# Performance work log

Hardware: AMD Instinct MI355X
Metric: run time of the kernel (lower is better)

Reference implementation:

```python
import jax, jax.numpy as jnp
import numpy as np

EPS = 1e-5

def conv2d(x, w, b, pad):
    # x: [B,C,H,W], w: [O,I,kh,kw] (OIHW), b: [O]
    y = jax.lax.conv_general_dilated(x, w, (1, 1), [(pad, pad), (pad, pad)],
                                     dimension_numbers=('NCHW', 'OIHW', 'NCHW'))
    return y + b[None, :, None, None]

def bn(x, g, b, m, v):
    # eval-mode BatchNorm2d
    scale = (g / jnp.sqrt(v + EPS))[None, :, None, None]
    return (x - m[None, :, None, None]) * scale + b[None, :, None, None]


def setup_inputs() -> dict:
    key = jax.random.key(0)
    ks = jax.random.split(key, 16)
    B, C, H, W = 2, 64, 64, 64
    Cq = C // 8
    f = lambda k, shp, s=0.05: jax.random.normal(k, shp, dtype=jnp.float32) * s
    return {
        'x': jax.random.normal(ks[0], (B, C, H, W), dtype=jnp.float32),
        'sW': f(ks[1], (C, C, 3, 3)), 'sb': f(ks[2], (C,)),
        's_g': jnp.ones((C,), jnp.float32), 's_b': jnp.zeros((C,), jnp.float32),
        's_m': jnp.zeros((C,), jnp.float32), 's_v': jnp.ones((C,), jnp.float32),
        'cW': f(ks[3], (C, C, 3, 3)), 'cb': f(ks[4], (C,)),
        'c_g': jnp.ones((C,), jnp.float32), 'c_b': jnp.zeros((C,), jnp.float32),
        'c_m': jnp.zeros((C,), jnp.float32), 'c_v': jnp.ones((C,), jnp.float32),
        'qW': f(ks[5], (Cq, C, 1, 1)), 'qb': f(ks[6], (Cq,)),
        'kW': f(ks[7], (Cq, C, 1, 1)), 'kb': f(ks[8], (Cq,)),
        'vW': f(ks[9], (C, C, 1, 1)), 'vb': f(ks[10], (C,)),
        'oW': f(ks[11], (C, C, 1, 1)), 'ob': f(ks[12], (C,)),
        's_gamma': jnp.array([0.5], jnp.float32),
        'c_gamma': jnp.array([0.5], jnp.float32),
    }


def reference(x, sW, sb, s_g, s_b, s_m, s_v, cW, cb, c_g, c_b, c_m, c_v,
              qW, qb, kW, kb, vW, vb, oW, ob, s_gamma, c_gamma):
    # ---- spatial attention branch ----
    s_x = jax.nn.relu(bn(conv2d(x, sW, sb, 1), s_g, s_b, s_m, s_v))  # [B,C,H,W]
    B, C, H, W = s_x.shape
    HW = H * W
    q = conv2d(x, qW, qb, 0).reshape(B, -1, HW)  # [B, C/8, HW]
    k = conv2d(x, kW, kb, 0).reshape(B, -1, HW)  # [B, C/8, HW]
    v = conv2d(x, vW, vb, 0).reshape(B, C, HW)   # [B, C,   HW]
    # aff[b,i,j] = q_i . k_j ; softmax over j (unscaled, per original)
    A = jax.nn.softmax(jnp.einsum('bdi,bdj->bij', q, k), axis=-1)  # [B,HW,HW]
    sa = jnp.einsum('bcj,bij->bci', v, A).reshape(B, C, H, W)
    sa_map = s_gamma[0] * sa + s_x
    # ---- channel attention branch ----
    c_x = jax.nn.relu(bn(conv2d(x, cW, cb, 1), c_g, c_b, c_m, c_v))  # [B,C,H,W]
    fmap = c_x.reshape(B, C, HW)
    Ac = jnp.einsum('bin,bjn->bij', fmap, fmap)  # [B,C,C]
    Ac = jax.nn.softmax(jnp.max(Ac, axis=-1, keepdims=True) - Ac, axis=-1)
    ca = jnp.einsum('bij,bjn->bin', Ac, fmap).reshape(B, C, H, W)
    ca_map = c_gamma[0] * ca + c_x
    # ---- fuse + output adaptor ----
    return conv2d(sa_map + ca_map, oW, ob, 0)
```

## Files before the change

### kernel.cpp

```cpp
#include <hip/hip_runtime.h>

#define HW 4096

typedef __attribute__((ext_vector_type(8)))  short short8;
typedef __attribute__((ext_vector_type(16))) float float16;

__device__ __forceinline__ unsigned short f2bf(float f) {
    unsigned u = __float_as_uint(f);
    u += 0x7fffu + ((u >> 16) & 1u);
    return (unsigned short)(u >> 16);
}

__global__ __launch_bounds__(256) void k_wprep(
    const float* __restrict__ sW, const float* __restrict__ cW,
    const float* __restrict__ sb, const float* __restrict__ cb,
    const float* __restrict__ s_g, const float* __restrict__ s_b,
    const float* __restrict__ s_m, const float* __restrict__ s_v,
    const float* __restrict__ c_g, const float* __restrict__ c_b,
    const float* __restrict__ c_m, const float* __restrict__ c_v,
    const float* __restrict__ oW,
    unsigned short* __restrict__ Wa, float* __restrict__ scsh,
    float* __restrict__ oWTg)
{
    int bx = blockIdx.x;
    int t = threadIdx.x;
    if (bx < 18) {
        int which = bx / 9, khw = bx % 9;
        const float* W = which ? cW : sW;
#pragma unroll
        for (int i = 0; i < 16; i++) {
            int idx = t + 256 * i;
            int oc = idx >> 6, ic = idx & 63;
            float v = W[(size_t)(oc * 64 + ic) * 9 + khw];
            Wa[((size_t)(which * 9 + khw) * 64 + oc) * 64 + ic] = f2bf(v);
        }
        if (bx == 0 && t < 128) {
            int wh = t >> 6, oc = t & 63;
            const float* g  = wh ? c_g : s_g;
            const float* bb = wh ? c_b : s_b;
            const float* m  = wh ? c_m : s_m;
            const float* vv = wh ? c_v : s_v;
            const float* cbias = wh ? cb : sb;
            float scale = g[oc] * rsqrtf(vv[oc] + 1e-5f);
            scsh[wh * 128 + oc]      = scale;
            scsh[wh * 128 + 64 + oc] = (cbias[oc] - m[oc]) * scale + bb[oc];
        }
    } else {
#pragma unroll
        for (int k = 0; k < 16; k++) {
            int idx = t + 256 * k;
            int c = idx >> 6, o = idx & 63;
            oWTg[idx] = oW[(size_t)o * 64 + c];
        }
    }
}

__global__ __launch_bounds__(256, 3) void k_conv_qkv(
    const float* __restrict__ x, const unsigned short* __restrict__ Wa,
    const float* __restrict__ scsh,
    const float* __restrict__ qW, const float* __restrict__ qb,
    const float* __restrict__ kW, const float* __restrict__ kb,
    const float* __restrict__ vW, const float* __restrict__ vb,
    float* __restrict__ sx, float* __restrict__ cx,
    unsigned short* __restrict__ qT, unsigned short* __restrict__ kT,
    unsigned short* __restrict__ vB)
{
    __shared__ unsigned short xs[3 * 8 * 66 * 8];
    int bx = blockIdx.x;
    int t = threadIdx.x;

    if (bx < 256) {
        int which = bx >> 7;
        int b     = (bx >> 6) & 1;
        int row   = bx & 63;
        const float* xb = x + (size_t)(b * 64) * HW;

#pragma unroll
        for (int it = 0; it < 6; it++) {
            int idx  = t + 256 * it;
            int col4 = idx & 15;
            int icp  = (idx >> 4) & 31;
            int lr   = idx >> 9;
            int ir   = row - 1 + lr;
            float fa[4] = {0.f, 0.f, 0.f, 0.f};
            float fb[4] = {0.f, 0.f, 0.f, 0.f};
            if (ir >= 0 && ir < 64) {
                const float* p0 = xb + (size_t)(icp * 2) * HW + ir * 64 + col4 * 4;
                float4 v0 = *(const float4*)p0;
                float4 v1 = *(const float4*)(p0 + HW);
                fa[0] = v0.x; fa[1] = v0.y; fa[2] = v0.z; fa[3] = v0.w;
                fb[0] = v1.x; fb[1] = v1.y; fb[2] = v1.z; fb[3] = v1.w;
            }
            int icg = icp >> 2, io = icp & 3;
#pragma unroll
            for (int j = 0; j < 4; j++) {
                unsigned pack = (unsigned)f2bf(fa[j]) | ((unsigned)f2bf(fb[j]) << 16);
                *(unsigned*)&xs[(((lr * 8 + icg) * 66 + col4 * 4 + j + 1) * 8) + io * 2] = pack;
            }
        }
        if (t < 192) {
            int pair = t & 3;
            int colsel = (t >> 2) & 1;
            int rg = t >> 3;
            *(unsigned*)&xs[((rg * 66 + colsel * 65) * 8) + pair * 2] = 0u;
        }
        __syncthreads();

        int lane = t & 63, w = t >> 6;
        int l31 = lane & 31, half = lane >> 5;
        int colh = w & 1;
        int m0   = (w >> 1) * 32;
        int c    = colh * 32 + l31;

        float16 acc;
#pragma unroll
        for (int i = 0; i < 16; i++) acc[i] = 0.f;

        const unsigned short* Wbase =
            Wa + ((size_t)which * 9) * 4096 + (size_t)(m0 + l31) * 64 + half * 8;

#pragma unroll
        for (int khw = 0; khw < 9; khw++) {
            const int kh = khw / 3, kw = khw % 3;
#pragma unroll
            for (int icq = 0; icq < 4; icq++) {
                short8 af = *(const short8*)(Wbase + (size_t)khw * 4096 + icq * 16);
                const unsigned short* bp =
                    &xs[((kh * 8 + icq * 2 + half) * 66 + kw) * 8];
                short8 bf = *(const short8*)(bp + (size_t)c * 8);
                acc = __builtin_amdgcn_mfma_f32_32x32x16_bf16(af, bf, acc, 0, 0, 0);
            }
        }

        float* out = (which ? cx : sx) + (size_t)(b * 64) * HW;
        const float* sc = scsh + which * 128;
        int hwbase = row * 64 + c;
#pragma unroll
        for (int r = 0; r < 16; r++) {
            int oc = m0 + (r & 3) + 8 * (r >> 2) + 4 * half;
            float s  = sc[oc];
            float sh = sc[64 + oc];
            out[(size_t)oc * HW + hwbase] = fmaxf(acc[r] * s + sh, 0.f);
        }
    } else {
        int ubx = bx - 256;
        int b = ubx / 80, rem = ubx % 80;
        int chunk = rem / 5, g = rem % 5;
        int hw = chunk * 256 + t;
        const float* xb = x + (size_t)(b * 64) * HW + hw;

        float acc[16];
#pragma unroll
        for (int u = 0; u < 16; u++) acc[u] = 0.f;

        if (g == 0) {
            for (int ic = 0; ic < 64; ic++) {
                float xv = xb[ic * HW];
#pragma unroll
                for (int u = 0; u < 8; u++) acc[u]     += qW[u * 64 + ic] * xv;
#pragma unroll
                for (int u = 0; u < 8; u++) acc[8 + u] += kW[u * 64 + ic] * xv;
            }
            short8 qv, kv;
#pragma unroll
            for (int u = 0; u < 8; u++) qv[u] = (short)f2bf(acc[u] + qb[u]);
#pragma unroll
            for (int u = 0; u < 8; u++) kv[u] = (short)f2bf(acc[8 + u] + kb[u]);
            *(short8*)(qT + ((size_t)(b * HW) + hw) * 8) = qv;
            *(short8*)(kT + ((size_t)(b * HW) + hw) * 8) = kv;
        } else {
            int c0 = (g - 1) * 16;
            for (int ic = 0; ic < 64; ic++) {
                float xv = xb[ic * HW];
#pragma unroll
                for (int u = 0; u < 16; u++) acc[u] += vW[(c0 + u) * 64 + ic] * xv;
            }
            int m  = hw & 15;
            int sg = (m & 3) | ((m & 4) << 1) | ((m & 8) >> 1);
            size_t base = ((size_t)(b * 256) + (hw >> 4)) * 1024 + sg;
#pragma unroll
            for (int u = 0; u < 16; u++)
                vB[base + (size_t)(c0 + u) * 16] = f2bf(acc[u] + vb[c0 + u]);
        }
    }
}

union SmemKB {
    struct { float o_sh[4][64][33]; float den_sh[4][32]; } a;
    float slab[64][68];
};

__global__ __launch_bounds__(256, 4) void k_attn_gram(
    const unsigned short* __restrict__ qT, const unsigned short* __restrict__ kT,
    const unsigned short* __restrict__ vB, const float* __restrict__ cx,
    float* __restrict__ Opart, float* __restrict__ denp,
    float* __restrict__ Gpart)
{
    __shared__ SmemKB sm;
    int bx = blockIdx.x;
    int t = threadIdx.x;

    if (bx < 1024) {
        int lane = t & 63, w = t >> 6;
        int half = lane >> 5, l31 = lane & 31;
        int b  = bx >> 9;
        int itile = (bx >> 2) & 127;
        int jh = bx & 3;
        int i0 = itile * 32;

        short8 qf;
        if (half == 0) {
            qf = *(const short8*)(qT + ((size_t)(b * HW) + i0 + l31) * 8);
        } else {
#pragma unroll
            for (int i = 0; i < 8; i++) qf[i] = 0;
        }

        float16 o0, o1;
#pragma unroll
        for (int i = 0; i < 16; i++) { o0[i] = 0.f; o1[i] = 0.f; }
        float denr = 0.f;

        const unsigned short* kTb = kT + (size_t)(b * HW) * 8;
        const unsigned short* vBb = vB + (size_t)b * (256 * 1024);

        for (int tile = 0; tile < 8; tile++) {
            int j0 = jh * 1024 + w * 256 + tile * 32;
            int g0 = j0 >> 4;

            short8 kf;
            if (half == 0) {
                kf = *(const short8*)(kTb + (size_t)(j0 + l31) * 8);
            } else {
#pragma unroll
                for (int i = 0; i < 8; i++) kf[i] = 0;
            }

            float16 z;
#pragma unroll
            for (int i = 0; i < 16; i++) z[i] = 0.f;
            float16 s = __builtin_amdgcn_mfma_f32_32x32x16_bf16(kf, qf, z, 0, 0, 0);

            float pr[16];
#pragma unroll
            for (int r = 0; r < 16; r++) {
                pr[r] = __expf(s[r]);
                denr += pr[r];
            }
            short8 pa0, pa1;
#pragma unroll
            for (int r = 0; r < 8; r++) {
                pa0[r] = (short)f2bf(pr[r]);
                pa1[r] = (short)f2bf(pr[8 + r]);
            }

            const unsigned short* vg0 = vBb + (size_t)g0 * 1024 + half * 8;
            short8 v00 = *(const short8*)(vg0 + (size_t)l31 * 16);
            short8 v01 = *(const short8*)(vg0 + (size_t)(32 + l31) * 16);
            short8 v10 = *(const short8*)(vg0 + 1024 + (size_t)l31 * 16);
            short8 v11 = *(const short8*)(vg0 + 1024 + (size_t)(32 + l31) * 16);

            o0 = __builtin_amdgcn_mfma_f32_32x32x16_bf16(pa0, v00, o0, 0, 0, 0);
            o1 = __builtin_amdgcn_mfma_f32_32x32x16_bf16(pa0, v01, o1, 0, 0, 0);
            o0 = __builtin_amdgcn_mfma_f32_32x32x16_bf16(pa1, v10, o0, 0, 0, 0);
            o1 = __builtin_amdgcn_mfma_f32_32x32x16_bf16(pa1, v11, o1, 0, 0, 0);
        }

        float dfull = denr + __shfl_xor(denr, 32);
        if (half == 0) sm.a.den_sh[w][l31] = dfull;
#pragma unroll
        for (int r = 0; r < 16; r++) {
            int il = (r & 3) + 8 * (r >> 2) + 4 * half;
            sm.a.o_sh[w][l31][il]      = o0[r];
            sm.a.o_sh[w][32 + l31][il] = o1[r];
        }
        __syncthreads();

        int i  = t & 31;
        int cg = t >> 5;
        if (cg == 0)
            denp[jh * 8192 + b * 4096 + i0 + i] =
                sm.a.den_sh[0][i] + sm.a.den_sh[1][i] +
                sm.a.den_sh[2][i] + sm.a.den_sh[3][i];
#pragma unroll
        for (int u = 0; u < 8; u++) {
            int c = cg * 8 + u;
            float sv = sm.a.o_sh[0][c][i] + sm.a.o_sh[1][c][i]
                     + sm.a.o_sh[2][c][i] + sm.a.o_sh[3][c][i];
            Opart[((size_t)(jh * 2 + b) * 64 + c) * HW + i0 + i] = sv;
        }
    } else {
        int gbx = bx - 1024;
        int b = gbx >> 5, slice = gbx & 31;
        int i0 = (t & 15) * 4, j0c = (t >> 4) * 4;
        float acc[4][4] = {};
#pragma unroll
        for (int ch = 0; ch < 2; ch++) {
            int hwb = slice * 128 + ch * 64;
            __syncthreads();
#pragma unroll
            for (int it = 0; it < 16; it++) {
                int idx = t + 256 * it;
                int hw = idx & 63, c = idx >> 6;
                sm.slab[hw][c] = cx[(size_t)(b * 64 + c) * HW + hwb + hw];
            }
            __syncthreads();
#pragma unroll 8
            for (int hw = 0; hw < 64; hw++) {
                float4 ai = *(const float4*)&sm.slab[hw][i0];
                float4 aj = *(const float4*)&sm.slab[hw][j0c];
                acc[0][0] += ai.x * aj.x; acc[0][1] += ai.x * aj.y;
                acc[0][2] += ai.x * aj.z; acc[0][3] += ai.x * aj.w;
                acc[1][0] += ai.y * aj.x; acc[1][1] += ai.y * aj.y;
                acc[1][2] += ai.y * aj.z; acc[1][3] += ai.y * aj.w;
                acc[2][0] += ai.z * aj.x; acc[2][1] += ai.z * aj.y;
                acc[2][2] += ai.z * aj.z; acc[2][3] += ai.z * aj.w;
                acc[3][0] += ai.w * aj.x; acc[3][1] += ai.w * aj.y;
                acc[3][2] += ai.w * aj.z; acc[3][3] += ai.w * aj.w;
            }
        }
        float* Gb = Gpart + ((size_t)(b * 32 + slice)) * 4096;
#pragma unroll
        for (int ii = 0; ii < 4; ii++)
            *(float4*)&Gb[(size_t)(i0 + ii) * 64 + j0c] =
                make_float4(acc[ii][0], acc[ii][1], acc[ii][2], acc[ii][3]);
    }
}

__global__ __launch_bounds__(256) void k_csoft(
    const float* __restrict__ Gpart, float* __restrict__ AcsT)
{
    int r = blockIdx.x * 4 + (threadIdx.x >> 6);
    int b = r >> 6, i = r & 63;
    int j = threadIdx.x & 63;

    const float* Gp = Gpart + (size_t)(b * 32) * 4096 + i * 64 + j;
    float a = 0.f;
#pragma unroll 8
    for (int sl = 0; sl < 32; sl++)
        a += Gp[(size_t)sl * 4096];

    float mn = a;
    mn = fminf(mn, __shfl_xor(mn, 1));
    mn = fminf(mn, __shfl_xor(mn, 2));
    mn = fminf(mn, __shfl_xor(mn, 4));
    mn = fminf(mn, __shfl_xor(mn, 8));
    mn = fminf(mn, __shfl_xor(mn, 16));
    mn = fminf(mn, __shfl_xor(mn, 32));
    float p = __expf(mn - a);
    float s = p;
    s += __shfl_xor(s, 1);
    s += __shfl_xor(s, 2);
    s += __shfl_xor(s, 4);
    s += __shfl_xor(s, 8);
    s += __shfl_xor(s, 16);
    s += __shfl_xor(s, 32);
    AcsT[(size_t)b * 4096 + j * 64 + i] = p / s;
}

__global__ __launch_bounds__(256) void k_fuse_out(
    const float* __restrict__ Opart, const float* __restrict__ denp,
    const float* __restrict__ sx,    const float* __restrict__ cx,
    const float* __restrict__ AcsT,
    const float* __restrict__ oWTg,  const float* __restrict__ ob,
    const float* __restrict__ s_gamma, const float* __restrict__ c_gamma,
    float* __restrict__ out)
{
    __shared__ float A_sh[64][68];
    __shared__ float cxs[64][33];
    __shared__ float f_sh[64][33];
    __shared__ float oWT[64][68];

    int bx = blockIdx.x;
    int b = bx >> 7, chunk = bx & 127;
    int px0 = chunk * 32;
    int t = threadIdx.x;
    float sgam = s_gamma[0], cgam = c_gamma[0];

#pragma unroll
    for (int k = 0; k < 16; k++) {
        int idx = t + 256 * k;
        int j = idx >> 6, i = idx & 63;
        A_sh[j][i] = AcsT[(size_t)b * 4096 + idx];
        oWT[j][i]  = oWTg[idx];
    }
#pragma unroll
    for (int k = 0; k < 8; k++) {
        int idx = t + 256 * k;
        int c = idx >> 5, px = idx & 31;
        size_t o = (size_t)(b * 64 + c) * HW + px0 + px;
        float cv = cx[o];
        cxs[c][px] = cv;
        float dd = denp[b * 4096 + px0 + px]
                 + denp[8192  + b * 4096 + px0 + px]
                 + denp[16384 + b * 4096 + px0 + px]
                 + denp[24576 + b * 4096 + px0 + px];
        float O = Opart[((size_t)(0 + b) * 64 + c) * HW + px0 + px]
                + Opart[((size_t)(2 + b) * 64 + c) * HW + px0 + px]
                + Opart[((size_t)(4 + b) * 64 + c) * HW + px0 + px]
                + Opart[((size_t)(6 + b) * 64 + c) * HW + px0 + px];
        f_sh[c][px] = sgam * (O / dd) + sx[o] + cv;
    }
    __syncthreads();

    {
        int px = t & 31, cg = t >> 5;
        int c0 = cg * 8;
        float ca[8] = {};
        for (int j = 0; j < 64; j++) {
            float xv = cxs[j][px];
            float4 a0 = *(const float4*)&A_sh[j][c0];
            float4 a1 = *(const float4*)&A_sh[j][c0 + 4];
            ca[0] += a0.x * xv; ca[1] += a0.y * xv;
            ca[2] += a0.z * xv; ca[3] += a0.w * xv;
            ca[4] += a1.x * xv; ca[5] += a1.y * xv;
            ca[6] += a1.z * xv; ca[7] += a1.w * xv;
        }
#pragma unroll
        for (int u = 0; u < 8; u++)
            f_sh[c0 + u][px] += cgam * ca[u];
    }
    __syncthreads();

    {
        int px = t & 31, og = t >> 5;
        int o0 = og * 8;
        float acc[8] = {};
        for (int c = 0; c < 64; c++) {
            float fv = f_sh[c][px];
            float4 a0 = *(const float4*)&oWT[c][o0];
            float4 a1 = *(const float4*)&oWT[c][o0 + 4];
            acc[0] += a0.x * fv; acc[1] += a0.y * fv;
            acc[2] += a0.z * fv; acc[3] += a0.w * fv;
            acc[4] += a1.x * fv; acc[5] += a1.y * fv;
            acc[6] += a1.z * fv; acc[7] += a1.w * fv;
        }
#pragma unroll
        for (int u = 0; u < 8; u++) {
            int o = o0 + u;
            out[(size_t)(b * 64 + o) * HW + px0 + px] = acc[u] + ob[o];
        }
    }
}

extern "C" void kernel_launch(void* const* d_in, const int* in_sizes, int n_in,
                              void* d_out, int out_size, void* d_ws, size_t ws_size,
                              hipStream_t stream)
{
    const float* x    = (const float*)d_in[0];
    const float* sW   = (const float*)d_in[1];
    const float* sb   = (const float*)d_in[2];
    const float* s_g  = (const float*)d_in[3];
    const float* s_b  = (const float*)d_in[4];
    const float* s_m  = (const float*)d_in[5];
    const float* s_v  = (const float*)d_in[6];
    const float* cW   = (const float*)d_in[7];
    const float* cb   = (const float*)d_in[8];
    const float* c_g  = (const float*)d_in[9];
    const float* c_b  = (const float*)d_in[10];
    const float* c_m  = (const float*)d_in[11];
    const float* c_v  = (const float*)d_in[12];
    const float* qW   = (const float*)d_in[13];
    const float* qb   = (const float*)d_in[14];
    const float* kW   = (const float*)d_in[15];
    const float* kb   = (const float*)d_in[16];
    const float* vW   = (const float*)d_in[17];
    const float* vb   = (const float*)d_in[18];
    const float* oW   = (const float*)d_in[19];
    const float* ob   = (const float*)d_in[20];
    const float* s_gamma = (const float*)d_in[21];
    const float* c_gamma = (const float*)d_in[22];

    float* ws    = (float*)d_ws;
    float* sx    = ws;
    float* cx    = ws + 524288;
    float* Opart = ws + 1048576;
    float* denp  = ws + 3145728;
    float* AcsT  = ws + 3178496;
    float* Gpart = ws + 3186688;
    float* oWTg  = ws + 3448832;
    float* scsh  = ws + 3452928;
    unsigned short* us = (unsigned short*)(ws + 3453184);
    unsigned short* qT = us;
    unsigned short* kT = us + 65536;
    unsigned short* vB = us + 131072;
    unsigned short* Wa = us + 655360;

    k_wprep<<<19, 256, 0, stream>>>(sW, cW, sb, cb, s_g, s_b, s_m, s_v,
                                    c_g, c_b, c_m, c_v, oW, Wa, scsh, oWTg);
    k_conv_qkv<<<416, 256, 0, stream>>>(x, Wa, scsh, qW, qb, kW, kb, vW, vb,
                                        sx, cx, qT, kT, vB);
    k_attn_gram<<<1088, 256, 0, stream>>>(qT, kT, vB, cx, Opart, denp, Gpart);
    k_csoft<<<32, 256, 0, stream>>>(Gpart, AcsT);
    k_fuse_out<<<256, 256, 0, stream>>>(Opart, denp, sx, cx, AcsT,
                                        oWTg, ob, s_gamma, c_gamma, (float*)d_out);
}
```

Baseline: 160.8 us.

## Fuse channel softmax into output kernel and reorder gram blocks first

Removes the separate channel-softmax kernel. Each output block now sums the gram partials itself and computes the 64x64 softmax in shared memory. The gram blocks are halved in count (16 slices of 256 pixels each) and moved to the front of the combined grid so they start first, and shared memory in the output kernel is unioned to fit the raw gram tile. This saves one kernel launch and a global round trip, but all 256 output blocks now redo the same partial reduction and softmax.

```diff
diff --git a/kernel.cpp b/kernel.cpp
--- a/kernel.cpp
+++ b/kernel.cpp
@@ -200,103 +200,13 @@
     int bx = blockIdx.x;
     int t = threadIdx.x;
 
-    if (bx < 1024) {
-        int lane = t & 63, w = t >> 6;
-        int half = lane >> 5, l31 = lane & 31;
-        int b  = bx >> 9;
-        int itile = (bx >> 2) & 127;
-        int jh = bx & 3;
-        int i0 = itile * 32;
-
-        short8 qf;
-        if (half == 0) {
-            qf = *(const short8*)(qT + ((size_t)(b * HW) + i0 + l31) * 8);
-        } else {
-#pragma unroll
-            for (int i = 0; i < 8; i++) qf[i] = 0;
-        }
-
-        float16 o0, o1;
-#pragma unroll
-        for (int i = 0; i < 16; i++) { o0[i] = 0.f; o1[i] = 0.f; }
-        float denr = 0.f;
-
-        const unsigned short* kTb = kT + (size_t)(b * HW) * 8;
-        const unsigned short* vBb = vB + (size_t)b * (256 * 1024);
-
-        for (int tile = 0; tile < 8; tile++) {
-            int j0 = jh * 1024 + w * 256 + tile * 32;
-            int g0 = j0 >> 4;
-
-            short8 kf;
-            if (half == 0) {
-                kf = *(const short8*)(kTb + (size_t)(j0 + l31) * 8);
-            } else {
-#pragma unroll
-                for (int i = 0; i < 8; i++) kf[i] = 0;
-            }
-
-            float16 z;
-#pragma unroll
-            for (int i = 0; i < 16; i++) z[i] = 0.f;
-            float16 s = __builtin_amdgcn_mfma_f32_32x32x16_bf16(kf, qf, z, 0, 0, 0);
-
-            float pr[16];
-#pragma unroll
-            for (int r = 0; r < 16; r++) {
-                pr[r] = __expf(s[r]);
-                denr += pr[r];
-            }
-            short8 pa0, pa1;
-#pragma unroll
-            for (int r = 0; r < 8; r++) {
-                pa0[r] = (short)f2bf(pr[r]);
-                pa1[r] = (short)f2bf(pr[8 + r]);
-            }
-
-            const unsigned short* vg0 = vBb + (size_t)g0 * 1024 + half * 8;
-            short8 v00 = *(const short8*)(vg0 + (size_t)l31 * 16);
-            short8 v01 = *(const short8*)(vg0 + (size_t)(32 + l31) * 16);
-            short8 v10 = *(const short8*)(vg0 + 1024 + (size_t)l31 * 16);
-            short8 v11 = *(const short8*)(vg0 + 1024 + (size_t)(32 + l31) * 16);
-
-            o0 = __builtin_amdgcn_mfma_f32_32x32x16_bf16(pa0, v00, o0, 0, 0, 0);
-            o1 = __builtin_amdgcn_mfma_f32_32x32x16_bf16(pa0, v01, o1, 0, 0, 0);
-            o0 = __builtin_amdgcn_mfma_f32_32x32x16_bf16(pa1, v10, o0, 0, 0, 0);
-            o1 = __builtin_amdgcn_mfma_f32_32x32x16_bf16(pa1, v11, o1, 0, 0, 0);
-        }
-
-        float dfull = denr + __shfl_xor(denr, 32);
-        if (half == 0) sm.a.den_sh[w][l31] = dfull;
-#pragma unroll
-        for (int r = 0; r < 16; r++) {
-            int il = (r & 3) + 8 * (r >> 2) + 4 * half;
-            sm.a.o_sh[w][l31][il]      = o0[r];
-            sm.a.o_sh[w][32 + l31][il] = o1[r];
-        }
-        __syncthreads();
-
-        int i  = t & 31;
-        int cg = t >> 5;
-        if (cg == 0)
-            denp[jh * 8192 + b * 4096 + i0 + i] =
-                sm.a.den_sh[0][i] + sm.a.den_sh[1][i] +
-                sm.a.den_sh[2][i] + sm.a.den_sh[3][i];
-#pragma unroll
-        for (int u = 0; u < 8; u++) {
-            int c = cg * 8 + u;
-            float sv = sm.a.o_sh[0][c][i] + sm.a.o_sh[1][c][i]
-                     + sm.a.o_sh[2][c][i] + sm.a.o_sh[3][c][i];
-            Opart[((size_t)(jh * 2 + b) * 64 + c) * HW + i0 + i] = sv;
-        }
-    } else {
-        int gbx = bx - 1024;
-        int b = gbx >> 5, slice = gbx & 31;
+    if (bx < 32) {
+        int b = bx >> 4, slice = bx & 15;
         int i0 = (t & 15) * 4, j0c = (t >> 4) * 4;
         float acc[4][4] = {};
 #pragma unroll
-        for (int ch = 0; ch < 2; ch++) {
-            int hwb = slice * 128 + ch * 64;
+        for (int ch = 0; ch < 4; ch++) {
+            int hwb = slice * 256 + ch * 64;
             __syncthreads();
 #pragma unroll
             for (int it = 0; it < 16; it++) {
@@ -319,57 +229,117 @@
                 acc[3][2] += ai.w * aj.z; acc[3][3] += ai.w * aj.w;
             }
         }
-        float* Gb = Gpart + ((size_t)(b * 32 + slice)) * 4096;
+        float* Gb = Gpart + ((size_t)(b * 16 + slice)) * 4096;
 #pragma unroll
         for (int ii = 0; ii < 4; ii++)
             *(float4*)&Gb[(size_t)(i0 + ii) * 64 + j0c] =
                 make_float4(acc[ii][0], acc[ii][1], acc[ii][2], acc[ii][3]);
+    } else {
+        int bx2 = bx - 32;
+        int lane = t & 63, w = t >> 6;
+        int half = lane >> 5, l31 = lane & 31;
+        int b  = bx2 >> 9;
+        int itile = (bx2 >> 2) & 127;
+        int jh = bx2 & 3;
+        int i0 = itile * 32;
+
+        short8 qf;
+        if (half == 0) {
+            qf = *(const short8*)(qT + ((size_t)(b * HW) + i0 + l31) * 8);
+        } else {
+#pragma unroll
+            for (int i = 0; i < 8; i++) qf[i] = 0;
+        }
+
+        float16 o0, o1;
+#pragma unroll
+        for (int i = 0; i < 16; i++) { o0[i] = 0.f; o1[i] = 0.f; }
+        float denr = 0.f;
+
+        const unsigned short* kTb = kT + (size_t)(b * HW) * 8;
+        const unsigned short* vBb = vB + (size_t)b * (256 * 1024);
+
+        for (int tile = 0; tile < 8; tile++) {
+            int j0 = jh * 1024 + w * 256 + tile * 32;
+            int g0 = j0 >> 4;
+
+            short8 kf;
+            if (half == 0) {
+                kf = *(const short8*)(kTb + (size_t)(j0 + l31) * 8);
+            } else {
+#pragma unroll
+                for (int i = 0; i < 8; i++) kf[i] = 0;
+            }
+
+            float16 z;
+#pragma unroll
+            for (int i = 0; i < 16; i++) z[i] = 0.f;
+            float16 s = __builtin_amdgcn_mfma_f32_32x32x16_bf16(kf, qf, z, 0, 0, 0);
+
+            float pr[16];
+#pragma unroll
+            for (int r = 0; r < 16; r++) {
+                pr[r] = __expf(s[r]);
+                denr += pr[r];
+            }
+            short8 pa0, pa1;
+#pragma unroll
+            for (int r = 0; r < 8; r++) {
+                pa0[r] = (short)f2bf(pr[r]);
+                pa1[r] = (short)f2bf(pr[8 + r]);
+            }
+
+            const unsigned short* vg0 = vBb + (size_t)g0 * 1024 + half * 8;
+            short8 v00 = *(const short8*)(vg0 + (size_t)l31 * 16);
+            short8 v01 = *(const short8*)(vg0 + (size_t)(32 + l31) * 16);
+            short8 v10 = *(const short8*)(vg0 + 1024 + (size_t)l31 * 16);
+            short8 v11 = *(const short8*)(vg0 + 1024 + (size_t)(32 + l31) * 16);
+
+            o0 = __builtin_amdgcn_mfma_f32_32x32x16_bf16(pa0, v00, o0, 0, 0, 0);
+            o1 = __builtin_amdgcn_mfma_f32_32x32x16_bf16(pa0, v01, o1, 0, 0, 0);
+            o0 = __builtin_amdgcn_mfma_f32_32x32x16_bf16(pa1, v10, o0, 0, 0, 0);
+            o1 = __builtin_amdgcn_mfma_f32_32x32x16_bf16(pa1, v11, o1, 0, 0, 0);
+        }
+
+        float dfull = denr + __shfl_xor(denr, 32);
+        if (half == 0) sm.a.den_sh[w][l31] = dfull;
+#pragma unroll
+        for (int r = 0; r < 16; r++) {
+            int il = (r & 3) + 8 * (r >> 2) + 4 * half;
+            sm.a.o_sh[w][l31][il]      = o0[r];
+            sm.a.o_sh[w][32 + l31][il] = o1[r];
+        }
+        __syncthreads();
+
+        int i  = t & 31;
+        int cg = t >> 5;
+        if (cg == 0)
+            denp[jh * 8192 + b * 4096 + i0 + i] =
+                sm.a.den_sh[0][i] + sm.a.den_sh[1][i] +
+                sm.a.den_sh[2][i] + sm.a.den_sh[3][i];
+#pragma unroll
+        for (int u = 0; u < 8; u++) {
+            int c = cg * 8 + u;
+            float sv = sm.a.o_sh[0][c][i] + sm.a.o_sh[1][c][i]
+                     + sm.a.o_sh[2][c][i] + sm.a.o_sh[3][c][i];
+            Opart[((size_t)(jh * 2 + b) * 64 + c) * HW + i0 + i] = sv;
+        }
     }
 }
 
-__global__ __launch_bounds__(256) void k_csoft(
-    const float* __restrict__ Gpart, float* __restrict__ AcsT)
-{
-    int r = blockIdx.x * 4 + (threadIdx.x >> 6);
-    int b = r >> 6, i = r & 63;
-    int j = threadIdx.x & 63;
-
-    const float* Gp = Gpart + (size_t)(b * 32) * 4096 + i * 64 + j;
-    float a = 0.f;
-#pragma unroll 8
-    for (int sl = 0; sl < 32; sl++)
-        a += Gp[(size_t)sl * 4096];
-
-    float mn = a;
-    mn = fminf(mn, __shfl_xor(mn, 1));
-    mn = fminf(mn, __shfl_xor(mn, 2));
-    mn = fminf(mn, __shfl_xor(mn, 4));
-    mn = fminf(mn, __shfl_xor(mn, 8));
-    mn = fminf(mn, __shfl_xor(mn, 16));
-    mn = fminf(mn, __shfl_xor(mn, 32));
-    float p = __expf(mn - a);
-    float s = p;
-    s += __shfl_xor(s, 1);
-    s += __shfl_xor(s, 2);
-    s += __shfl_xor(s, 4);
-    s += __shfl_xor(s, 8);
-    s += __shfl_xor(s, 16);
-    s += __shfl_xor(s, 32);
-    AcsT[(size_t)b * 4096 + j * 64 + i] = p / s;
-}
-
 __global__ __launch_bounds__(256) void k_fuse_out(
+    const float* __restrict__ Gpart,
     const float* __restrict__ Opart, const float* __restrict__ denp,
     const float* __restrict__ sx,    const float* __restrict__ cx,
-    const float* __restrict__ AcsT,
     const float* __restrict__ oWTg,  const float* __restrict__ ob,
     const float* __restrict__ s_gamma, const float* __restrict__ c_gamma,
     float* __restrict__ out)
 {
     __shared__ float A_sh[64][68];
-    __shared__ float cxs[64][33];
-    __shared__ float f_sh[64][33];
-    __shared__ float oWT[64][68];
+    __shared__ union {
+        float A_raw[64][68];
+        struct { float cxs[64][33]; float f_sh[64][33]; float oWT[64][68]; } s;
+    } u;
 
     int bx = blockIdx.x;
     int b = bx >> 7, chunk = bx & 127;
@@ -377,12 +347,48 @@
     int t = threadIdx.x;
     float sgam = s_gamma[0], cgam = c_gamma[0];
 
+    const float* Gb = Gpart + (size_t)(b * 16) * 4096;
 #pragma unroll
     for (int k = 0; k < 16; k++) {
         int idx = t + 256 * k;
-        int j = idx >> 6, i = idx & 63;
-        A_sh[j][i] = AcsT[(size_t)b * 4096 + idx];
-        oWT[j][i]  = oWTg[idx];
+        float a = 0.f;
+#pragma unroll
+        for (int sl = 0; sl < 16; sl++)
+            a += Gb[(size_t)sl * 4096 + idx];
+        u.A_raw[idx >> 6][idx & 63] = a;
+    }
+    __syncthreads();
+
+    {
+        int w = t >> 6, j = t & 63;
+#pragma unroll
+        for (int r = 0; r < 16; r++) {
+            int i = w * 16 + r;
+            float a = u.A_raw[i][j];
+            float mn = a;
+            mn = fminf(mn, __shfl_xor(mn, 1));
+            mn = fminf(mn, __shfl_xor(mn, 2));
+            mn = fminf(mn, __shfl_xor(mn, 4));
+            mn = fminf(mn, __shfl_xor(mn, 8));
+            mn = fminf(mn, __shfl_xor(mn, 16));
+            mn = fminf(mn, __shfl_xor(mn, 32));
+            float p = __expf(mn - a);
+            float s = p;
+            s += __shfl_xor(s, 1);
+            s += __shfl_xor(s, 2);
+            s += __shfl_xor(s, 4);
+            s += __shfl_xor(s, 8);
+            s += __shfl_xor(s, 16);
+            s += __shfl_xor(s, 32);
+            A_sh[j][i] = p / s;
+        }
+    }
+    __syncthreads();
+
+#pragma unroll
+    for (int k = 0; k < 16; k++) {
+        int idx = t + 256 * k;
+        u.s.oWT[idx >> 6][idx & 63] = oWTg[idx];
     }
 #pragma unroll
     for (int k = 0; k < 8; k++) {
@@ -390,7 +396,7 @@
         int c = idx >> 5, px = idx & 31;
         size_t o = (size_t)(b * 64 + c) * HW + px0 + px;
         float cv = cx[o];
-        cxs[c][px] = cv;
+        u.s.cxs[c][px] = cv;
         float dd = denp[b * 4096 + px0 + px]
                  + denp[8192  + b * 4096 + px0 + px]
                  + denp[16384 + b * 4096 + px0 + px]
@@ -399,7 +405,7 @@
                 + Opart[((size_t)(2 + b) * 64 + c) * HW + px0 + px]
                 + Opart[((size_t)(4 + b) * 64 + c) * HW + px0 + px]
                 + Opart[((size_t)(6 + b) * 64 + c) * HW + px0 + px];
-        f_sh[c][px] = sgam * (O / dd) + sx[o] + cv;
+        u.s.f_sh[c][px] = sgam * (O / dd) + sx[o] + cv;
     }
     __syncthreads();
 
@@ -408,7 +414,7 @@
         int c0 = cg * 8;
         float ca[8] = {};
         for (int j = 0; j < 64; j++) {
-            float xv = cxs[j][px];
+            float xv = u.s.cxs[j][px];
             float4 a0 = *(const float4*)&A_sh[j][c0];
             float4 a1 = *(const float4*)&A_sh[j][c0 + 4];
             ca[0] += a0.x * xv; ca[1] += a0.y * xv;
@@ -417,8 +423,8 @@
             ca[6] += a1.z * xv; ca[7] += a1.w * xv;
         }
 #pragma unroll
-        for (int u = 0; u < 8; u++)
-            f_sh[c0 + u][px] += cgam * ca[u];
+        for (int uu = 0; uu < 8; uu++)
+            u.s.f_sh[c0 + uu][px] += cgam * ca[uu];
     }
     __syncthreads();
 
@@ -427,18 +433,18 @@
         int o0 = og * 8;
         float acc[8] = {};
         for (int c = 0; c < 64; c++) {
-            float fv = f_sh[c][px];
-            float4 a0 = *(const float4*)&oWT[c][o0];
-            float4 a1 = *(const float4*)&oWT[c][o0 + 4];
+            float fv = u.s.f_sh[c][px];
+            float4 a0 = *(const float4*)&u.s.oWT[c][o0];
+            float4 a1 = *(const float4*)&u.s.oWT[c][o0 + 4];
             acc[0] += a0.x * fv; acc[1] += a0.y * fv;
             acc[2] += a0.z * fv; acc[3] += a0.w * fv;
             acc[4] += a1.x * fv; acc[5] += a1.y * fv;
             acc[6] += a1.z * fv; acc[7] += a1.w * fv;
         }
 #pragma unroll
-        for (int u = 0; u < 8; u++) {
-            int o = o0 + u;
-            out[(size_t)(b * 64 + o) * HW + px0 + px] = acc[u] + ob[o];
+        for (int uu = 0; uu < 8; uu++) {
+            int o = o0 + uu;
+            out[(size_t)(b * 64 + o) * HW + px0 + px] = acc[uu] + ob[o];
         }
     }
 }
@@ -476,11 +482,10 @@
     float* cx    = ws + 524288;
     float* Opart = ws + 1048576;
     float* denp  = ws + 3145728;
-    float* AcsT  = ws + 3178496;
-    float* Gpart = ws + 3186688;
-    float* oWTg  = ws + 3448832;
-    float* scsh  = ws + 3452928;
-    unsigned short* us = (unsigned short*)(ws + 3453184);
+    float* Gpart = ws + 3178496;
+    float* oWTg  = ws + 3309568;
+    float* scsh  = ws + 3313664;
+    unsigned short* us = (unsigned short*)(ws + 3313920);
     unsigned short* qT = us;
     unsigned short* kT = us + 65536;
     unsigned short* vB = us + 131072;
@@ -490,8 +495,7 @@
                                     c_g, c_b, c_m, c_v, oW, Wa, scsh, oWTg);
     k_conv_qkv<<<416, 256, 0, stream>>>(x, Wa, scsh, qW, qb, kW, kb, vW, vb,
                                         sx, cx, qT, kT, vB);
-    k_attn_gram<<<1088, 256, 0, stream>>>(qT, kT, vB, cx, Opart, denp, Gpart);
-    k_csoft<<<32, 256, 0, stream>>>(Gpart, AcsT);
-    k_fuse_out<<<256, 256, 0, stream>>>(Opart, denp, sx, cx, AcsT,
+    k_attn_gram<<<1056, 256, 0, stream>>>(qT, kT, vB, cx, Opart, denp, Gpart);
+    k_fuse_out<<<256, 256, 0, stream>>>(Gpart, Opart, denp, sx, cx,
                                         oWTg, ob, s_gamma, c_gamma, (float*)d_out);
 }
```

Result: slower. 165.7 us (+3.1%).
